# Kernel optimization log

Hardware: AMD Instinct MI355X
Metric: run time of the kernel (lower is better)

The kernel has to match this reference:

```python
import jax, jax.numpy as jnp
import numpy as np


def setup_inputs() -> dict:
    key = jax.random.key(0)
    ks = jax.random.split(key, 5)
    B, T, C, H, E = 8, 2048, 1024, 2048, 8
    n_layer = 12
    x = jax.random.normal(ks[0], (B, T, C), dtype=jnp.float32)
    w_router = jax.random.normal(ks[1], (C, E), dtype=jnp.float32) * 0.02
    w_c_fc = jax.random.normal(ks[2], (E, C, H), dtype=jnp.float32) * 0.02
    w_gate = jax.random.normal(ks[3], (E, C, H), dtype=jnp.float32) * 0.02
    w_c_proj = jax.random.normal(ks[4], (E, H, C), dtype=jnp.float32) * (0.02 * (2 * n_layer) ** -0.5)
    return {
        "x": x, "w_router": w_router, "w_c_fc": w_c_fc,
        "w_gate": w_gate, "w_c_proj": w_c_proj,
        "top_k": 2, "n_experts": E, "expert_capacity": 640,
    }


def reference(x, w_router, w_c_fc, w_gate, w_c_proj, top_k, n_experts, expert_capacity):
    B, T, C = x.shape
    # ---- router ----
    gate_logits = jnp.einsum('btc,ce->bte', x, w_router)
    gate_probs = jax.nn.softmax(gate_logits, axis=-1)  # (B,T,E)

    # ---- per-batch top-k dispatch (cumsum slot assignment + scatter) ----
    def dispatch(xb, pb):
        # xb: (T,C), pb: (T,E)
        topk_p, topk_i = jax.lax.top_k(pb, top_k)              # (T,k)
        ei = jnp.swapaxes(topk_i, 0, 1).ravel()                # (k*T,) k-major
        oh = jax.nn.one_hot(ei, n_experts, dtype=jnp.int32)    # (k*T,E)
        pos = jnp.cumsum(oh, axis=0) * oh - 1                  # slot within expert
        pos = jnp.swapaxes(pos.reshape(top_k, T, n_experts), 0, 1).max(axis=2)  # (T,k)
        ei = jnp.swapaxes(ei.reshape(top_k, T), 0, 1)          # (T,k)
        buf = jnp.zeros((n_experts, expert_capacity, C), dtype=xb.dtype)
        xr = jnp.repeat(xb, top_k, axis=0)                     # (T*k,C) token-major
        buf = buf.at[ei.ravel(), pos.ravel()].set(xr)          # overflow slots dropped
        return topk_p, pos, ei, buf

    topk_p, pos, ei, buf = jax.vmap(dispatch)(x, gate_probs)   # buf: (B,E,cap,C)

    # ---- batched expert SwiGLU GEMMs ----
    ein = jnp.swapaxes(buf, 0, 1).reshape(n_experts, B * expert_capacity, C)
    h = jnp.einsum('eti,eih->eth', ein, w_c_fc)
    g = jax.nn.silu(jnp.einsum('eti,eih->eth', ein, w_gate))
    o = jnp.einsum('eth,eho->eto', g * h, w_c_proj)
    eo = jnp.swapaxes(o.reshape(n_experts, B, expert_capacity, C), 0, 1)  # (B,E,cap,C)

    # ---- weighted combine gather ----
    def combine(eo_b, i_b, p_b, pr_b):
        sel = eo_b[i_b, p_b]                                   # (T,k,C)
        return jnp.sum(pr_b[..., None] * sel, axis=1)          # (T,C)

    y = jax.vmap(combine)(eo, ei, pos, topk_p)                 # (B,T,C)
    return y
```

## Files before the change

kernel.cpp:

```cpp
#include <hip/hip_runtime.h>
#include <stdint.h>

#define B_   8
#define T_   2048
#define C_   1024
#define H_   2048
#define E_   8
#define CAP_ 640
#define RPE_ (B_*CAP_)
#define BT_  (B_*T_)

typedef __attribute__((ext_vector_type(8))) short bf16x8;
typedef __attribute__((ext_vector_type(4))) float f32x4;

static __device__ __forceinline__ unsigned short f2bf(float f){
  union { float f; uint32_t u; } a; a.f = f;
  uint32_t u = a.u;
  uint32_t r = (u + 0x7FFFu + ((u >> 16) & 1u)) >> 16;
  return (unsigned short)r;
}

#define GLD16(gp, lp) __builtin_amdgcn_global_load_lds( \
    (__attribute__((address_space(1))) void*)(gp), \
    (__attribute__((address_space(3))) void*)(lp), 16, 0, 0)

#define VMW(N) asm volatile("s_waitcnt vmcnt(" #N ")" ::: "memory")
#define FENCE  asm volatile("" ::: "memory")
#define BARS   do { FENCE; __builtin_amdgcn_s_barrier(); __builtin_amdgcn_sched_barrier(0); } while(0)
#define BARE   do { __builtin_amdgcn_sched_barrier(0); FENCE; __builtin_amdgcn_s_barrier(); FENCE; } while(0)

#define LDA(H) do { \
  _Pragma("unroll") for (int ks_=0; ks_<2; ++ks_) \
  _Pragma("unroll") for (int f_=0; f_<4; ++f_) \
    pa[ks_][f_] = *(const bf16x8*)(bufc + (H)*16384u + aRow + (unsigned)f_*2048u + cc[ks_]); \
} while(0)
#define LDB(PB, H) do { \
  _Pragma("unroll") for (int ks_=0; ks_<2; ++ks_) \
  _Pragma("unroll") for (int n_=0; n_<2; ++n_) \
    PB[ks_][n_] = *(const bf16x8*)(bufc + 32768u + (H)*16384u + bRow + (unsigned)n_*2048u + cc[ks_]); \
} while(0)
#define MM16(Q, PB) do { \
  __builtin_amdgcn_s_setprio(1); \
  _Pragma("unroll") for (int ks_=0; ks_<2; ++ks_) \
  _Pragma("unroll") for (int f_=0; f_<4; ++f_) \
  _Pragma("unroll") for (int n_=0; n_<2; ++n_) \
    acc[Q][f_][n_] = __builtin_amdgcn_mfma_f32_16x16x32_bf16(pa[ks_][f_], PB[ks_][n_], acc[Q][f_][n_], 0,0,0); \
  __builtin_amdgcn_s_setprio(0); \
} while(0)

#define STG_A(H, T1) do { \
  unsigned kb_ = (unsigned)(T1)*128u; \
  unsigned db_ = ((unsigned)(T1)&1u)*65536u + (H)*16384u; \
  GLD16(pA##H##0 + kb_, lds + db_ + d0); \
  GLD16(pA##H##1 + kb_, lds + db_ + 8192u + d0); \
} while(0)
#define STG_B(H, T1) do { \
  unsigned kb_ = (unsigned)(T1)*128u; \
  unsigned db_ = ((unsigned)(T1)&1u)*65536u + 32768u + (H)*16384u; \
  GLD16(pB##H##0 + kb_, lds + db_ + d0); \
  GLD16(pB##H##1 + kb_, lds + db_ + 8192u + d0); \
} while(0)

__global__ __launch_bounds__(256) void router_kernel(
    const float* __restrict__ x, const float* __restrict__ wr,
    unsigned short* __restrict__ xbf, float* __restrict__ probs2, int* __restrict__ idx2)
{
  int bt = blockIdx.x;
  int tid = threadIdx.x;
  const float4 v = ((const float4*)(x + (size_t)bt*C_))[tid];
  ushort4 u;
  u.x = f2bf(v.x); u.y = f2bf(v.y); u.z = f2bf(v.z); u.w = f2bf(v.w);
  ((ushort4*)(xbf + (size_t)bt*C_))[tid] = u;

  double p[8];
  #pragma unroll
  for (int e=0;e<8;e++) p[e]=0.0;
  const float xv[4] = {v.x, v.y, v.z, v.w};
  #pragma unroll
  for (int j=0;j<4;j++){
    int c = tid*4+j;
    const float* wrow = wr + c*8;
    #pragma unroll
    for (int e=0;e<8;e++) p[e] += (double)xv[j] * (double)wrow[e];
  }
  __shared__ double red[8][256];
  #pragma unroll
  for (int e=0;e<8;e++) red[e][tid] = p[e];
  __syncthreads();
  for (int s=128; s>0; s>>=1){
    if (tid < s){
      #pragma unroll
      for (int e=0;e<8;e++) red[e][tid] += red[e][tid+s];
    }
    __syncthreads();
  }
  if (tid==0){
    double lg[8];
    #pragma unroll
    for (int e=0;e<8;e++) lg[e]=red[e][0];
    double mx = lg[0];
    #pragma unroll
    for (int e=1;e<8;e++) if (lg[e]>mx) mx=lg[e];
    double s=0.0, ex[8];
    #pragma unroll
    for (int e=0;e<8;e++){ ex[e]=exp(lg[e]-mx); s+=ex[e]; }
    int i1=0; double b1=ex[0];
    #pragma unroll
    for (int e=1;e<8;e++) if (ex[e]>b1){ b1=ex[e]; i1=e; }
    int i2=-1; double b2=-1.0;
    #pragma unroll
    for (int e=0;e<8;e++) if (e!=i1 && ex[e]>b2){ b2=ex[e]; i2=e; }
    probs2[bt*2+0] = (float)(b1/s);
    probs2[bt*2+1] = (float)(b2/s);
    idx2[bt*2+0] = i1;
    idx2[bt*2+1] = i2;
  }
}

__global__ __launch_bounds__(256) void transp_fcg_kernel(
    const float* __restrict__ fc, const float* __restrict__ gate,
    unsigned short* __restrict__ dst)
{
  __shared__ float t[32][33];
  int e = blockIdx.z;
  int n0 = blockIdx.x*32, k0 = blockIdx.y*32;
  int tx = threadIdx.x & 31, ty = threadIdx.x >> 5;
  #pragma unroll
  for (int sel=0; sel<2; ++sel){
    const float* s = (sel ? gate : fc) + ((size_t)e*C_ + k0)*H_ + n0;
    #pragma unroll
    for (int i=0;i<32;i+=8) t[ty+i][tx] = s[(size_t)(ty+i)*H_ + tx];
    __syncthreads();
    #pragma unroll
    for (int i=0;i<32;i+=8){
      int jj = ty+i;
      int drow = n0*2 + ((jj & 16) << 1) + sel*16 + (jj & 15);
      dst[((size_t)e*4096 + drow)*1024 + k0 + tx] = f2bf(t[tx][jj]);
    }
    __syncthreads();
  }
}

__global__ __launch_bounds__(256) void transp_kernel(
    const float* __restrict__ src, unsigned short* __restrict__ dst, int K, int N)
{
  __shared__ float t[32][33];
  int e = blockIdx.z;
  int n0 = blockIdx.x*32, k0 = blockIdx.y*32;
  int tx = threadIdx.x & 31, ty = threadIdx.x >> 5;
  const float* s = src + ((size_t)e*K + k0)*N + n0;
  #pragma unroll
  for (int i=0;i<32;i+=8) t[ty+i][tx] = s[(size_t)(ty+i)*N + tx];
  __syncthreads();
  unsigned short* d = dst + ((size_t)e*N + n0)*K + k0;
  #pragma unroll
  for (int i=0;i<32;i+=8) d[(size_t)(ty+i)*K + tx] = f2bf(t[tx][ty+i]);
}

__global__ void scan_kernel(const int* __restrict__ idx2, int* __restrict__ pos, int* __restrict__ cnt)
{
  int b = blockIdx.x, lane = threadIdx.x;
  unsigned long long below = (lane == 0) ? 0ull : (~0ull >> (64 - lane));
  int base = 0;
  for (int k=0;k<2;k++){
    for (int c0=0;c0<T_;c0+=64){
      int t = c0 + lane;
      int e = idx2[((b*T_ + t)<<1) + k];
      unsigned long long mym = 0; int addv = 0;
      #pragma unroll
      for (int ee=0; ee<8; ++ee){
        unsigned long long m = __ballot(e == ee);
        if (ee == e) mym = m;
        if (lane == ee) addv = __popcll(m);
      }
      int mybase = __shfl(base, e, 64);
      pos[((b*T_+t)<<1)+k] = mybase + __popcll(mym & below);
      base += addv;
    }
  }
  if (lane < 8) cnt[b*8 + lane] = (base < CAP_) ? base : CAP_;
}

__global__ void offsets_kernel(const int* __restrict__ cnt, int* __restrict__ off, int* __restrict__ Me)
{
  int e = threadIdx.x;
  if (e < 8){
    int s = 0;
    for (int b=0;b<8;b++){ off[e*8+b] = s; s += cnt[b*8+e]; }
    Me[e] = s;
  }
}

__global__ void fill_kernel(const int* __restrict__ idx2, const int* __restrict__ pos,
                            const int* __restrict__ off, const float* __restrict__ probs2,
                            int* __restrict__ token_src, float* __restrict__ row_prob)
{
  int a = blockIdx.x*256 + threadIdx.x;
  if (a >= BT_*2) return;
  int bt = a >> 1, k = a & 1;
  int b = bt >> 11;
  int e = idx2[bt*2+k];
  int p = pos[bt*2+k];
  if (p < CAP_){
    int r = e*RPE_ + off[e*8+b] + p;
    token_src[r] = bt;
    row_prob[r] = probs2[bt*2+k];
  }
}

__global__ __launch_bounds__(512, 2) void gemm1_kernel(
    const unsigned short* __restrict__ xbf,
    const unsigned short* __restrict__ wifcg,
    const int* __restrict__ token_src,
    const int* __restrict__ Me,
    unsigned short* __restrict__ act,
    int e0)
{
  const int ez = blockIdx.z, e = e0 + ez, mt = blockIdx.y, nt = blockIdx.x;
  const int M = Me[e];
  if (mt*256 >= M) return;

  __shared__ __align__(16) unsigned char lds[131072];

  const int tid = threadIdx.x;
  const int w = tid >> 6, l = tid & 63;
  const int wm = w >> 2, wn = w & 3;
  const int l15 = l & 15, g0 = l >> 4;
  const unsigned d0 = (unsigned)tid * 16u;

  const int srow0 = tid >> 3, c0 = tid & 7;
  const unsigned scb = (unsigned)((c0 ^ (srow0 & 7)) * 16);
  const unsigned char* gA = (const unsigned char*)xbf;
  const unsigned char* gB = (const unsigned char*)wifcg;
  const int abase = e*RPE_ + mt*256;
  const unsigned char* pA00 = gA + (size_t)token_src[abase +       srow0]*2048u + scb;
  const unsigned char* pA01 = gA + (size_t)token_src[abase +  64 + srow0]*2048u + scb;
  const unsigned char* pA10 = gA + (size_t)token_src[abase + 128 + srow0]*2048u + scb;
  const unsigned char* pA11 = gA + (size_t)token_src[abase + 192 + srow0]*2048u + scb;
  const size_t bbase = (size_t)(ez*4096 + nt*256 + srow0);
  const unsigned char* pB00 = gB + (bbase +   0)*2048u + scb;
  const unsigned char* pB01 = gB + (bbase +  64)*2048u + scb;
  const unsigned char* pB10 = gB + (bbase + 128)*2048u + scb;
  const unsigned char* pB11 = gB + (bbase + 192)*2048u + scb;

  const unsigned aRow = (unsigned)((wm*64 + l15) * 128);
  const unsigned bRow = (unsigned)((wn*32 + l15) * 128);
  unsigned cc[2];
  cc[0] = (unsigned)(((0*4 + g0) ^ (l15 & 7)) * 16);
  cc[1] = (unsigned)(((1*4 + g0) ^ (l15 & 7)) * 16);

  f32x4 acc[4][4][2];
  #pragma unroll
  for (int p=0;p<4;++p)
    #pragma unroll
    for (int f=0;f<4;++f)
      #pragma unroll
      for (int n=0;n<2;++n) acc[p][f][n] = (f32x4){0.f,0.f,0.f,0.f};

  bf16x8 pa[2][4], pb0[2][2], pb1[2][2];

  STG_A(0,0); STG_B(0,0); STG_B(1,0); STG_A(1,0);
  VMW(4);
  FENCE; __builtin_amdgcn_s_barrier(); FENCE;

  const int NT = 16;
  for (int t = 0; t < NT-1; ++t){
    const unsigned char* bufc = lds + (unsigned)(t&1)*65536u;
    LDA(0); LDB(pb0,0); STG_A(0,t+1); VMW(4); BARS; MM16(0,pb0); BARE;
    LDB(pb1,1);         STG_B(0,t+1); VMW(4); BARS; MM16(1,pb1); BARE;
    LDA(1);             STG_B(1,t+1);         BARS; MM16(2,pb0); BARE;
                        STG_A(1,t+1); VMW(4); BARS; MM16(3,pb1); BARE;
  }
  {
    const unsigned char* bufc = lds + (unsigned)((NT-1)&1)*65536u;
    LDA(0); LDB(pb0,0); VMW(2); BARS; MM16(0,pb0); BARE;
    LDB(pb1,1);         VMW(0); BARS; MM16(1,pb1); BARE;
    LDA(1);                     BARS; MM16(2,pb0); BARE;
                                BARS; MM16(3,pb1); BARE;
  }

  const int r4 = (l >> 4) * 4;
  #pragma unroll
  for (int p=0;p<4;++p){
    const int ah = p>>1, bh = p&1;
    #pragma unroll
    for (int f=0;f<4;++f){
      const int grow = mt*256 + ah*128 + wm*64 + f*16 + r4;
      const int hcol = nt*128 + bh*64 + wn*16 + l15;
      #pragma unroll
      for (int r=0;r<4;++r){
        float h = acc[p][f][0][r];
        float gv = acc[p][f][1][r];
        float a = (gv / (1.f + __expf(-gv))) * h;
        act[((size_t)ez*RPE_ + grow + r)*(size_t)H_ + hcol] = f2bf(a);
      }
    }
  }
}

__global__ __launch_bounds__(512, 2) void gemm2_kernel(
    const unsigned short* __restrict__ act,
    const unsigned short* __restrict__ wprojT,
    const int* __restrict__ token_src,
    const float* __restrict__ row_prob,
    const int* __restrict__ Me,
    float* __restrict__ y,
    int e0)
{
  const int z = blockIdx.z, ez = z >> 1, ksl = z & 1;
  const int e = e0 + ez, mt = blockIdx.y, nt = blockIdx.x;
  const int M = Me[e];
  if (mt*256 >= M) return;

  __shared__ __align__(16) unsigned char lds[131072];

  const int tid = threadIdx.x;
  const int w = tid >> 6, l = tid & 63;
  const int wm = w >> 2, wn = w & 3;
  const int l15 = l & 15, g0 = l >> 4;
  const unsigned d0 = (unsigned)tid * 16u;

  const int srow0 = tid >> 3, c0 = tid & 7;
  const unsigned scb = (unsigned)((c0 ^ (srow0 & 7)) * 16) + (unsigned)ksl*2048u;
  const unsigned char* gA = (const unsigned char*)act;
  const unsigned char* gB = (const unsigned char*)wprojT;
  const size_t abase = (size_t)(ez*RPE_ + mt*256 + srow0);
  const unsigned char* pA00 = gA + (abase +   0)*4096u + scb;
  const unsigned char* pA01 = gA + (abase +  64)*4096u + scb;
  const unsigned char* pA10 = gA + (abase + 128)*4096u + scb;
  const unsigned char* pA11 = gA + (abase + 192)*4096u + scb;
  const size_t bbase = (size_t)(ez*C_ + nt*256 + srow0);
  const unsigned char* pB00 = gB + (bbase +   0)*4096u + scb;
  const unsigned char* pB01 = gB + (bbase +  64)*4096u + scb;
  const unsigned char* pB10 = gB + (bbase + 128)*4096u + scb;
  const unsigned char* pB11 = gB + (bbase + 192)*4096u + scb;

  const unsigned aRow = (unsigned)((wm*64 + l15) * 128);
  const unsigned bRow = (unsigned)((wn*32 + l15) * 128);
  unsigned cc[2];
  cc[0] = (unsigned)(((0*4 + g0) ^ (l15 & 7)) * 16);
  cc[1] = (unsigned)(((1*4 + g0) ^ (l15 & 7)) * 16);

  f32x4 acc[4][4][2];
  #pragma unroll
  for (int p=0;p<4;++p)
    #pragma unroll
    for (int f=0;f<4;++f)
      #pragma unroll
      for (int n=0;n<2;++n) acc[p][f][n] = (f32x4){0.f,0.f,0.f,0.f};

  bf16x8 pa[2][4], pb0[2][2], pb1[2][2];

  STG_A(0,0); STG_B(0,0); STG_B(1,0); STG_A(1,0);
  VMW(4);
  FENCE; __builtin_amdgcn_s_barrier(); FENCE;

  const int NT = 16;
  for (int t = 0; t < NT-1; ++t){
    const unsigned char* bufc = lds + (unsigned)(t&1)*65536u;
    LDA(0); LDB(pb0,0); STG_A(0,t+1); VMW(4); BARS; MM16(0,pb0); BARE;
    LDB(pb1,1);         STG_B(0,t+1); VMW(4); BARS; MM16(1,pb1); BARE;
    LDA(1);             STG_B(1,t+1);         BARS; MM16(2,pb0); BARE;
                        STG_A(1,t+1); VMW(4); BARS; MM16(3,pb1); BARE;
  }
  {
    const unsigned char* bufc = lds + (unsigned)((NT-1)&1)*65536u;
    LDA(0); LDB(pb0,0); VMW(2); BARS; MM16(0,pb0); BARE;
    LDB(pb1,1);         VMW(0); BARS; MM16(1,pb1); BARE;
    LDA(1);                     BARS; MM16(2,pb0); BARE;
                                BARS; MM16(3,pb1); BARE;
  }

  const int r4 = (l >> 4) * 4;
  #pragma unroll
  for (int p=0;p<4;++p){
    const int ah = p>>1, bh = p&1;
    #pragma unroll
    for (int f=0;f<4;++f){
      #pragma unroll
      for (int r=0;r<4;++r){
        const int rloc = mt*256 + ah*128 + wm*64 + f*16 + r4 + r;
        if (rloc < M){
          const int bt = token_src[e*RPE_ + rloc];
          const float pp = row_prob[e*RPE_ + rloc];
          float* yrow = y + (size_t)bt*C_;
          const int colb = nt*256 + bh*128 + wn*32 + l15;
          atomicAdd(yrow + colb,      pp * acc[p][f][0][r]);
          atomicAdd(yrow + colb + 16, pp * acc[p][f][1][r]);
        }
      }
    }
  }
}

extern "C" void kernel_launch(void* const* d_in, const int* in_sizes, int n_in,
                              void* d_out, int out_size, void* d_ws, size_t ws_size,
                              hipStream_t stream)
{
  const float* x   = (const float*)d_in[0];
  const float* wr  = (const float*)d_in[1];
  const float* wfc = (const float*)d_in[2];
  const float* wg  = (const float*)d_in[3];
  const float* wpj = (const float*)d_in[4];
  float* y = (float*)d_out;

  unsigned char* ws = (unsigned char*)d_ws;
  const size_t szXBF  = (size_t)BT_*C_*2;
  const size_t szFCGc = (size_t)2*4096*1024*2;
  const size_t szWPc  = (size_t)2*C_*H_*2;
  const size_t szFCGa = (size_t)E_*4096*1024*2;
  const size_t szWPa  = (size_t)E_*C_*H_*2;
  const size_t szMISC = 3*131072 + 2*(size_t)E_*RPE_*4 + 1024;

  const size_t need_small = szXBF + szFCGc + szWPc + (size_t)2*RPE_*H_*2 + szMISC;
  const size_t need_big2  = szXBF + szFCGa + szWPa  + (size_t)2*RPE_*H_*2 + szMISC;
  const size_t need_big4  = szXBF + szFCGa + szWPa  + (size_t)4*RPE_*H_*2 + szMISC;
  if (ws_size < need_small) return;
  const bool big4 = (ws_size >= need_big4);
  const bool big  = big4 || (ws_size >= need_big2);
  const int  ne   = big4 ? 4 : 2;

  const size_t szFCG = big ? szFCGa : szFCGc;
  const size_t szWP  = big ? szWPa  : szWPc;
  const size_t szACT = (size_t)ne*RPE_*H_*2;

  size_t oXBF = 0;
  size_t oFCG = oXBF + szXBF;
  size_t oWP  = oFCG + szFCG;
  size_t oACT = oWP  + szWP;
  size_t oM   = oACT + szACT;

  unsigned short* xbf    = (unsigned short*)(ws + oXBF);
  unsigned short* wifcg  = (unsigned short*)(ws + oFCG);
  unsigned short* wprojT = (unsigned short*)(ws + oWP);
  unsigned short* actc   = (unsigned short*)(ws + oACT);

  float* probs2    = (float*)(ws + oM);
  int*   idx2      = (int*)(ws + oM + 1*131072);
  int*   pos       = (int*)(ws + oM + 2*131072);
  int*   token_src = (int*)(ws + oM + 3*131072);
  float* row_prob  = (float*)(ws + oM + 3*131072 + (size_t)E_*RPE_*4);
  int*   cnt       = (int*)(ws + oM + 3*131072 + 2*(size_t)E_*RPE_*4);
  int*   off       = cnt + 64;
  int*   Me        = off + 64;

  hipMemsetAsync(y, 0, (size_t)out_size*4, stream);
  hipMemsetAsync(token_src, 0, (size_t)E_*RPE_*4, stream);

  router_kernel<<<BT_, 256, 0, stream>>>(x, wr, xbf, probs2, idx2);
  scan_kernel<<<B_, 64, 0, stream>>>(idx2, pos, cnt);
  offsets_kernel<<<1, 64, 0, stream>>>(cnt, off, Me);
  fill_kernel<<<(BT_*2+255)/256, 256, 0, stream>>>(idx2, pos, off, probs2, token_src, row_prob);

  if (big){
    transp_fcg_kernel<<<dim3(H_/32, C_/32, E_), 256, 0, stream>>>(wfc, wg, wifcg);
    transp_kernel<<<dim3(C_/32, H_/32, E_), 256, 0, stream>>>(wpj, wprojT, H_, C_);
  }

  for (int e0 = 0; e0 < E_; e0 += ne){
    unsigned short* wfcg_c = wifcg;
    unsigned short* wpj_c  = wprojT;
    if (big){
      wfcg_c = wifcg  + (size_t)e0*4096*1024;
      wpj_c  = wprojT + (size_t)e0*C_*H_;
    } else {
      transp_fcg_kernel<<<dim3(H_/32, C_/32, ne), 256, 0, stream>>>(
          wfc + (size_t)e0*C_*H_, wg + (size_t)e0*C_*H_, wifcg);
      transp_kernel<<<dim3(C_/32, H_/32, ne), 256, 0, stream>>>(
          wpj + (size_t)e0*H_*C_, wprojT, H_, C_);
    }
    gemm1_kernel<<<dim3(4096/256, RPE_/256, ne), 512, 0, stream>>>(
        xbf, wfcg_c, token_src, Me, actc, e0);
    gemm2_kernel<<<dim3(C_/256, RPE_/256, ne*2), 512, 0, stream>>>(
        actc, wpj_c, token_src, row_prob, Me, y, e0);
  }
}
```

Measured before the change: 843.3 us.

## Restructure gemm2 to 256x128 tiles with triple-buffered LDS and no split-K

The projection GEMM drops its 2-way split-K over H and instead uses 256x128 output tiles that loop over the full K with a three-stage LDS ring, so two tiles are prefetched ahead of compute. This halves the number of fp32 atomicAdds into y, since each output element is no longer written by two K-slices, and gives deeper load/compute overlap. In exchange each block holds half the accumulators and B-tile reuse per A load drops. LDS rises to 144KB per block, which may lower occupancy against the launch bound of 2 blocks per SM.

```diff
diff --git a/kernel.cpp b/kernel.cpp
--- a/kernel.cpp
+++ b/kernel.cpp
@@ -59,6 +59,19 @@
   unsigned db_ = ((unsigned)(T1)&1u)*65536u + 32768u + (H)*16384u; \
   GLD16(pB##H##0 + kb_, lds + db_ + d0); \
   GLD16(pB##H##1 + kb_, lds + db_ + 8192u + d0); \
+} while(0)
+
+#define STG2_A(H, T2, BI) do { \
+  unsigned kb_ = (unsigned)(T2)*128u; \
+  unsigned db_ = (unsigned)(BI)*49152u + (H)*16384u; \
+  GLD16(pA##H##0 + kb_, lds + db_ + d0); \
+  GLD16(pA##H##1 + kb_, lds + db_ + 8192u + d0); \
+} while(0)
+#define STG2_B(T2, BI) do { \
+  unsigned kb_ = (unsigned)(T2)*128u; \
+  unsigned db_ = (unsigned)(BI)*49152u + 32768u; \
+  GLD16(pB00 + kb_, lds + db_ + d0); \
+  GLD16(pB01 + kb_, lds + db_ + 8192u + d0); \
 } while(0)
 
 __global__ __launch_bounds__(256) void router_kernel(
@@ -307,12 +320,11 @@
     float* __restrict__ y,
     int e0)
 {
-  const int z = blockIdx.z, ez = z >> 1, ksl = z & 1;
-  const int e = e0 + ez, mt = blockIdx.y, nt = blockIdx.x;
+  const int ez = blockIdx.z, e = e0 + ez, mt = blockIdx.y, nt = blockIdx.x;
   const int M = Me[e];
   if (mt*256 >= M) return;
 
-  __shared__ __align__(16) unsigned char lds[131072];
+  __shared__ __align__(16) unsigned char lds[147456];
 
   const int tid = threadIdx.x;
   const int w = tid >> 6, l = tid & 63;
@@ -321,7 +333,7 @@
   const unsigned d0 = (unsigned)tid * 16u;
 
   const int srow0 = tid >> 3, c0 = tid & 7;
-  const unsigned scb = (unsigned)((c0 ^ (srow0 & 7)) * 16) + (unsigned)ksl*2048u;
+  const unsigned scb = (unsigned)((c0 ^ (srow0 & 7)) * 16);
   const unsigned char* gA = (const unsigned char*)act;
   const unsigned char* gB = (const unsigned char*)wprojT;
   const size_t abase = (size_t)(ez*RPE_ + mt*256 + srow0);
@@ -329,11 +341,9 @@
   const unsigned char* pA01 = gA + (abase +  64)*4096u + scb;
   const unsigned char* pA10 = gA + (abase + 128)*4096u + scb;
   const unsigned char* pA11 = gA + (abase + 192)*4096u + scb;
-  const size_t bbase = (size_t)(ez*C_ + nt*256 + srow0);
+  const size_t bbase = (size_t)(ez*C_ + nt*128 + srow0);
   const unsigned char* pB00 = gB + (bbase +   0)*4096u + scb;
   const unsigned char* pB01 = gB + (bbase +  64)*4096u + scb;
-  const unsigned char* pB10 = gB + (bbase + 128)*4096u + scb;
-  const unsigned char* pB11 = gB + (bbase + 192)*4096u + scb;
 
   const unsigned aRow = (unsigned)((wm*64 + l15) * 128);
   const unsigned bRow = (unsigned)((wn*32 + l15) * 128);
@@ -341,50 +351,52 @@
   cc[0] = (unsigned)(((0*4 + g0) ^ (l15 & 7)) * 16);
   cc[1] = (unsigned)(((1*4 + g0) ^ (l15 & 7)) * 16);
 
-  f32x4 acc[4][4][2];
-  #pragma unroll
-  for (int p=0;p<4;++p)
+  f32x4 acc[2][4][2];
+  #pragma unroll
+  for (int p=0;p<2;++p)
     #pragma unroll
     for (int f=0;f<4;++f)
       #pragma unroll
       for (int n=0;n<2;++n) acc[p][f][n] = (f32x4){0.f,0.f,0.f,0.f};
 
-  bf16x8 pa[2][4], pb0[2][2], pb1[2][2];
-
-  STG_A(0,0); STG_B(0,0); STG_B(1,0); STG_A(1,0);
-  VMW(4);
+  bf16x8 pa[2][4], pb[2][2];
+
+  STG2_A(0,0,0); STG2_B(0,0); STG2_A(1,0,0);
+  STG2_A(0,1,1); STG2_B(1,1); STG2_A(1,1,1);
+  VMW(8);
   FENCE; __builtin_amdgcn_s_barrier(); FENCE;
 
-  const int NT = 16;
-  for (int t = 0; t < NT-1; ++t){
-    const unsigned char* bufc = lds + (unsigned)(t&1)*65536u;
-    LDA(0); LDB(pb0,0); STG_A(0,t+1); VMW(4); BARS; MM16(0,pb0); BARE;
-    LDB(pb1,1);         STG_B(0,t+1); VMW(4); BARS; MM16(1,pb1); BARE;
-    LDA(1);             STG_B(1,t+1);         BARS; MM16(2,pb0); BARE;
-                        STG_A(1,t+1); VMW(4); BARS; MM16(3,pb1); BARE;
+  const int NT = 32;
+  for (int t = 0; t < NT-2; ++t){
+    const unsigned char* bufc = lds + (unsigned)(t%3)*49152u;
+    const int bi2 = (t+2)%3;
+    LDA(0); LDB(pb,0); STG2_A(0,t+2,bi2); STG2_B(t+2,bi2); VMW(10); BARS; MM16(0,pb); BARE;
+    LDA(1);            STG2_A(1,t+2,bi2);                  VMW(8);  BARS; MM16(1,pb); BARE;
   }
   {
-    const unsigned char* bufc = lds + (unsigned)((NT-1)&1)*65536u;
-    LDA(0); LDB(pb0,0); VMW(2); BARS; MM16(0,pb0); BARE;
-    LDB(pb1,1);         VMW(0); BARS; MM16(1,pb1); BARE;
-    LDA(1);                     BARS; MM16(2,pb0); BARE;
-                                BARS; MM16(3,pb1); BARE;
+    const unsigned char* bufc = lds + (unsigned)((NT-2)%3)*49152u;
+    LDA(0); LDB(pb,0); VMW(6); BARS; MM16(0,pb); BARE;
+    LDA(1);            VMW(2); BARS; MM16(1,pb); BARE;
+  }
+  {
+    const unsigned char* bufc = lds + (unsigned)((NT-1)%3)*49152u;
+    LDA(0); LDB(pb,0); VMW(0); BARS; MM16(0,pb); BARE;
+    LDA(1);                    BARS; MM16(1,pb); BARE;
   }
 
   const int r4 = (l >> 4) * 4;
   #pragma unroll
-  for (int p=0;p<4;++p){
-    const int ah = p>>1, bh = p&1;
+  for (int p=0;p<2;++p){
     #pragma unroll
     for (int f=0;f<4;++f){
       #pragma unroll
       for (int r=0;r<4;++r){
-        const int rloc = mt*256 + ah*128 + wm*64 + f*16 + r4 + r;
+        const int rloc = mt*256 + p*128 + wm*64 + f*16 + r4 + r;
         if (rloc < M){
           const int bt = token_src[e*RPE_ + rloc];
           const float pp = row_prob[e*RPE_ + rloc];
           float* yrow = y + (size_t)bt*C_;
-          const int colb = nt*256 + bh*128 + wn*32 + l15;
+          const int colb = nt*128 + wn*32 + l15;
           atomicAdd(yrow + colb,      pp * acc[p][f][0][r]);
           atomicAdd(yrow + colb + 16, pp * acc[p][f][1][r]);
         }
@@ -471,7 +483,7 @@
     }
     gemm1_kernel<<<dim3(4096/256, RPE_/256, ne), 512, 0, stream>>>(
         xbf, wfcg_c, token_src, Me, actc, e0);
-    gemm2_kernel<<<dim3(C_/256, RPE_/256, ne*2), 512, 0, stream>>>(
+    gemm2_kernel<<<dim3(C_/128, RPE_/256, ne), 512, 0, stream>>>(
         actc, wpj_c, token_src, row_prob, Me, y, e0);
   }
 }
```

Result: faster. 792.4 us (-6.0%).
